# Kernel optimization log

Hardware: AMD Instinct MI355X
Metric: run time of the kernel (lower is better)

The kernel has to match this reference:

```python
import jax, jax.numpy as jnp
import numpy as np

N_NODES = 50000
N_EDGES = 800000
MUL = 32                      # multiplicity of 0e and 1o in node_feats
AVG_NUM_NEIGHBORS = 16.0
INV_SQRT3 = 1.0 / np.sqrt(3.0)


def setup_inputs() -> dict:
    key = jax.random.key(0)
    ks = jax.random.split(key, 7)
    return {
        "node_feats": jax.random.normal(ks[0], (N_NODES, 4 * MUL), dtype=jnp.float32),
        "edge_attrs": jax.random.normal(ks[1], (N_EDGES, 4), dtype=jnp.float32),
        "senders": jax.random.randint(ks[2], (N_EDGES,), 0, N_NODES, dtype=jnp.int64) if jax.config.jax_enable_x64 else jax.random.randint(ks[2], (N_EDGES,), 0, N_NODES, dtype=jnp.int32),
        "receivers": jax.random.randint(ks[3], (N_EDGES,), 0, N_NODES, dtype=jnp.int32),
        "w_mlp0": jax.random.normal(ks[4], (1, 64), dtype=jnp.float32),
        "w_mlp1": jax.random.normal(ks[5], (64, 64), dtype=jnp.float32),
        "w_mlp2": jax.random.normal(ks[6], (64, 4 * MUL), dtype=jnp.float32),
    }


def reference(node_feats, edge_attrs, senders, receivers, w_mlp0, w_mlp1, w_mlp2):
    # node_feats layout: [N, MUL] scalars (0e) then [N, MUL*3] flattened vectors (1o)
    s = node_feats[:, :MUL]                          # [N, MUL]   32x0e
    v = node_feats[:, MUL:].reshape(-1, MUL, 3)      # [N, MUL,3] 32x1o

    # gather sender features per edge
    s_e = s[senders]                                 # [E, MUL]
    v_e = v[senders]                                 # [E, MUL, 3]

    ea0 = edge_attrs[:, :1]                          # [E,1]  1x0e
    ea1 = edge_attrs[:, 1:4]                         # [E,3]  1x1o

    # equivariant tensor product with edge_attrs.filter(drop='0e') = 1x1o,
    # keeping only target irreps (0e,1o):
    #   0e x 1o -> 1o : scalar * vector
    tp_1o = s_e[:, :, None] * ea1[:, None, :]        # [E, MUL, 3]
    #   1o x 1o -> 0e : dot / sqrt(3)  (component normalization)
    tp_0e = jnp.einsum('eci,ei->ec', v_e, ea1) * INV_SQRT3  # [E, MUL]

    # concatenate([msgs.filter(target), tp]).regroup() -> 64x0e + 64x1o
    scalars = jnp.concatenate([s_e, tp_0e], axis=1)          # [E, 2*MUL]
    vectors = jnp.concatenate([v_e, tp_1o], axis=1)          # [E, 2*MUL, 3]

    # MLP gate on scalar edge attrs (e3nn MLP: no bias, 1/sqrt(fan_in), swish)
    h = jax.nn.swish(ea0 @ w_mlp0 / jnp.sqrt(1.0))           # [E,64]
    h = jax.nn.swish(h @ w_mlp1 / jnp.sqrt(64.0))            # [E,64]
    mix = h @ w_mlp2 / jnp.sqrt(64.0)                        # [E, 4*MUL]

    n_sc = 2 * MUL
    scalars = scalars * mix[:, :n_sc]                        # gate 0e
    vectors = vectors * mix[:, n_sc:, None]                  # gate 1o (one scalar per vector)

    msgs = jnp.concatenate([scalars, vectors.reshape(vectors.shape[0], -1)], axis=1)  # [E, 8*MUL]

    # scatter-add messages to receivers
    out = jax.ops.segment_sum(msgs, receivers, num_segments=N_NODES)  # [N, 8*MUL]
    return out / jnp.sqrt(AVG_NUM_NEIGHBORS)
```

## Files before the change

### kernel.cpp

```cpp
#include <hip/hip_runtime.h>
#include <hip/hip_fp16.h>
#include <cstdint>

#define N_NODES   50000
#define FEAT      128
#define OUTF      256
#define MAX_EDGES 800000
#define CAP       64
#define INV_SQRT3 0.57735026918962576f
#define NW        (64 + 64*64 + 64*128)
#define TB_BLKS   ((N_NODES * 32 + 255) / 256)

__device__ float    g_wf[NW];
__device__ uint16_t g_lut16[65536 * 128];
__device__ uint16_t g_tbl[N_NODES * FEAT];
__device__ int      g_flags[4];
__device__ int      g_cnt[N_NODES];
__device__ uint2    g_slot[N_NODES * CAP];
__device__ unsigned char g_used[65536];

__device__ __forceinline__ float b2f(uint32_t b) {
    union { uint32_t u; float f; } v; v.u = b << 16; return v.f;
}
__device__ __forceinline__ uint32_t f2b_bits(float f) {
    union { float f; uint32_t u; } v; v.f = f;
    uint32_t u = v.u;
    u += 0x7fffu + ((u >> 16) & 1u);
    return u >> 16;
}
__device__ __forceinline__ float swishf(float x) {
    return x / (1.0f + __expf(-x));
}
__device__ __forceinline__ float sane(float x) {
    union { float f; uint32_t u; } v; v.f = x;
    return (((v.u >> 23) & 0xffu) >= 0x8Du) ? 0.0f : x;
}
__device__ __forceinline__ float loadf(const void* p, int i, int isbf) {
    return isbf ? b2f(((const uint16_t*)p)[i]) : ((const float*)p)[i];
}
__device__ __forceinline__ float h2f(uint32_t bits16) {
    return __half2float(__ushort_as_half((unsigned short)bits16));
}
__device__ __forceinline__ uint32_t f2h(float x) {
    return (uint32_t)__half_as_ushort(__float2half(x));
}

__global__ __launch_bounds__(256) void init_kernel(
    const void* nf, const void* ea, const void* w0, const void* w1, const void* w2,
    const int* snd, const int* rcv, int snd_force64, int n_edges)
{
    int bx = blockIdx.x, t = threadIdx.x;
    if (bx == 0) {
        __shared__ int viol[4];
        if (t < 4) viol[t] = 0;
        __syncthreads();
        {   int n = N_NODES * FEAT; int step = (n / 256) | 1;
            long long i = (long long)t * step;
            if (i < n) {
                uint32_t e = (((const uint16_t*)nf)[i] >> 7) & 0xffu;
                if (e > 140u) atomicOr(&viol[2], 1);
            } }
        {   int n = n_edges * 4; int step = (n / 256) | 1;
            long long i = (long long)t * step;
            if (i < n) {
                uint32_t e = (((const uint16_t*)ea)[i] >> 7) & 0xffu;
                if (e > 140u) atomicOr(&viol[3], 1);
            } }
        if (t < 64) {
            int i = 2 * t + 1;
            if (i < 2 * n_edges) {
                if (snd[i] != 0) atomicOr(&viol[0], 1);
                if (rcv[i] != 0) atomicOr(&viol[1], 1);
            }
        }
        __syncthreads();
        if (t == 0) {
            g_flags[0] = snd_force64 ? 1 : !viol[0];
            g_flags[1] = !viol[1];
            g_flags[2] = !viol[2];
            g_flags[3] = !viol[3];
        }
    } else if (bx <= 49) {
        __shared__ int wv[3];
        if (t < 3) wv[t] = 0;
        __syncthreads();
        if (t < 64) {
            uint32_t e = (((const uint16_t*)w0)[t] >> 7) & 0xffu;
            if (e > 140u) atomicOr(&wv[0], 1);
        }
        { int i = t * 17; if (i < 4096) {
            uint32_t e = (((const uint16_t*)w1)[i] >> 7) & 0xffu;
            if (e > 140u) atomicOr(&wv[1], 1); } }
        { int i = t * 33; if (i < 8192) {
            uint32_t e = (((const uint16_t*)w2)[i] >> 7) & 0xffu;
            if (e > 140u) atomicOr(&wv[2], 1); } }
        __syncthreads();
        int i = (bx - 1) * 256 + t;
        if (i < 64)             g_wf[i] = loadf(w0, i, !wv[0]);
        else if (i < 64 + 4096) g_wf[i] = loadf(w1, i - 64, !wv[1]);
        else if (i < NW)        g_wf[i] = loadf(w2, i - (64 + 4096), !wv[2]);
    } else if (bx <= 49 + TB_BLKS) {
        __shared__ int nv;
        if (t == 0) nv = 0;
        __syncthreads();
        {   int n = N_NODES * FEAT; int step = (n / 256) | 1;
            long long i = (long long)t * step;
            if (i < n) {
                uint32_t e = (((const uint16_t*)nf)[i] >> 7) & 0xffu;
                if (e > 140u) atomicOr(&nv, 1);
            } }
        __syncthreads();
        int f2l = !nv;
        int i = (bx - 50) * 256 + t;
        if (i < N_NODES * 32) {
            int node = i >> 5, c = i & 31;
            int rb = node * FEAT;
            float s  = loadf(nf, rb + c, f2l);
            float v0 = loadf(nf, rb + 32 + 3 * c + 0, f2l);
            float v1 = loadf(nf, rb + 32 + 3 * c + 1, f2l);
            float v2 = loadf(nf, rb + 32 + 3 * c + 2, f2l);
            uint32_t lo = f2h(s)  | (f2h(v0) << 16);
            uint32_t hi = f2h(v1) | (f2h(v2) << 16);
            ((uint2*)g_tbl)[i] = make_uint2(lo, hi);
        }
    } else {
        __shared__ int ev[3];
        if (t < 3) ev[t] = 0;
        __syncthreads();
        {   int n = n_edges * 4; int step = (n / 256) | 1;
            long long i = (long long)t * step;
            if (i < n) {
                uint32_t x = (((const uint16_t*)ea)[i] >> 7) & 0xffu;
                if (x > 140u) atomicOr(&ev[2], 1);
            } }
        if (t < 64) {
            int i = 2 * t + 1;
            if (i < 2 * n_edges) {
                if (snd[i] != 0) atomicOr(&ev[0], 1);
                if (rcv[i] != 0) atomicOr(&ev[1], 1);
            }
        }
        __syncthreads();
        int f0l = snd_force64 ? 1 : !ev[0];
        int f1l = !ev[1];
        int f3l = !ev[2];
        int e = (bx - 50 - TB_BLKS) * 256 + t;
        if (e < n_edges) {
            int ri = f1l ? rcv[2 * e] : rcv[e];
            ri = min(max(ri, 0), N_NODES - 1);
            uint32_t b0 = f3l ? (uint32_t)((const uint16_t*)ea)[4 * e]
                              : f2b_bits(((const float*)ea)[4 * e]);
            b0 &= 0xffffu;
            int s_ = f0l ? snd[2 * e] : snd[e];
            s_ = min(max(s_, 0), N_NODES - 1);
            g_used[b0] = 1;
            int p = atomicAdd(&g_cnt[ri], 1);
            if (p < CAP) g_slot[ri * CAP + p] = make_uint2(((uint32_t)s_ << 16) | b0, (uint32_t)e);
        }
    }
}

__global__ __launch_bounds__(256) void lut_kernel() {
    int w = blockIdx.x * 4 + (threadIdx.x >> 6);
    int lane = threadIdx.x & 63;
    int f = (lane < 16) ? (g_used[w + lane * 4096] != 0) : 0;
    unsigned long long mask = __ballot(f) & 0xffffull;
    if (!mask) return;
    const float* w1 = g_wf + 64;
    const float* w2 = g_wf + 64 + 4096;
    float w0l = g_wf[lane];
    while (mask) {
        int k = __builtin_ctzll(mask);
        mask &= mask - 1;
        int r = w + k * 4096;
        float x = b2f((uint32_t)r);
        float h0 = swishf(x * w0l);
        float a = 0.f;
        #pragma unroll 8
        for (int kk = 0; kk < 64; ++kk)
            a += __shfl(h0, kk, 64) * w1[kk * 64 + lane];
        float h1 = swishf(a * 0.125f);
        float a0 = 0.f, a1 = 0.f;
        #pragma unroll 8
        for (int kk = 0; kk < 64; ++kk) {
            float h1k = __shfl(h1, kk, 64);
            a0 += h1k * w2[kk * 128 + lane];
            a1 += h1k * w2[kk * 128 + 64 + lane];
        }
        float s1c = 0.125f * 0.25f;
        float s0c = (lane >= 32) ? s1c * INV_SQRT3 : s1c;
        float pa = sane(a0 * s0c);
        float pb = sane(a1 * s1c);
        float qa = __shfl_xor(pa, 32, 64);
        float qb = __shfl_xor(pb, 32, 64);
        if (lane < 32) {
            uint32_t lo = f2h(pa) | (f2h(qa) << 16);
            uint32_t hi = f2h(pb) | (f2h(qb) << 16);
            ((uint2*)(g_lut16 + (size_t)r * 128))[lane] = make_uint2(lo, hi);
        }
    }
}

__global__ __launch_bounds__(256) void gather_kernel(
    const void* __restrict__ ea, void* __restrict__ out)
{
    int wid = (blockIdx.x * 256 + threadIdx.x) >> 6;
    int lane = threadIdx.x & 63;
    if (wid >= N_NODES) return;
    int c = lane & 31;
    int half = lane >> 5;
    const int f2 = g_flags[2], f3 = g_flags[3];
    int deg = min(g_cnt[wid], CAP);
    if (lane == 0) g_cnt[wid] = 0;

    float o0 = 0.f, o1 = 0.f, o2 = 0.f, o3 = 0.f,
          o4 = 0.f, o5 = 0.f, o6 = 0.f, o7 = 0.f;

    uint32_t pk_p = 0;
    float ex_p = 0.f, ey_p = 0.f, ez_p = 0.f;
    if (lane < deg) {
        uint2 sl = g_slot[wid * CAP + lane];
        pk_p = sl.x;
        int e = (int)sl.y;
        if (f3) {
            uint2 w = ((const uint2*)ea)[e];
            ex_p = b2f(w.x >> 16);
            ey_p = b2f(w.y & 0xffffu);
            ez_p = b2f(w.y >> 16);
        } else {
            float4 w = ((const float4*)ea)[e];
            ex_p = w.y; ey_p = w.z; ez_p = w.w;
        }
    }

    const uint2* tbl = (const uint2*)g_tbl;

    for (int j = 0; j < deg; j += 4) {
        int jjA = j + half, jjB = j + 2 + half;
        float gA = (jjA < deg) ? 1.0f : 0.0f;
        float gB = (jjB < deg) ? 1.0f : 0.0f;
        int jxA = (jjA < deg) ? jjA : 0;
        int jxB = (jjB < deg) ? jjB : 0;

        uint32_t pkA = (uint32_t)__shfl((int)pk_p, jxA, 64);
        uint32_t pkB = (uint32_t)__shfl((int)pk_p, jxB, 64);
        float exA = __shfl(ex_p, jxA, 64), eyA = __shfl(ey_p, jxA, 64), ezA = __shfl(ez_p, jxA, 64);
        float exB = __shfl(ex_p, jxB, 64), eyB = __shfl(ey_p, jxB, 64), ezB = __shfl(ez_p, jxB, 64);

        uint2 mAu = ((const uint2*)(g_lut16 + (size_t)(pkA & 0xffffu) * 128))[c];
        uint2 mBu = ((const uint2*)(g_lut16 + (size_t)(pkB & 0xffffu) * 128))[c];
        uint2 hA = tbl[(size_t)(pkA >> 16) * 32 + c];
        uint2 hB = tbl[(size_t)(pkB >> 16) * 32 + c];

        float sA  = h2f(hA.x & 0xffffu), vA0 = h2f(hA.x >> 16);
        float vA1 = h2f(hA.y & 0xffffu), vA2 = h2f(hA.y >> 16);
        float sB  = h2f(hB.x & 0xffffu), vB0 = h2f(hB.x >> 16);
        float vB1 = h2f(hB.y & 0xffffu), vB2 = h2f(hB.y >> 16);

        {
            float m0 = h2f(mAu.x & 0xffffu) * gA, m1 = h2f(mAu.x >> 16) * gA;
            float m2 = h2f(mAu.y & 0xffffu) * gA, m3 = h2f(mAu.y >> 16) * gA;
            o0 += sA * m0;
            o1 += (vA0 * exA + vA1 * eyA + vA2 * ezA) * m1;
            o2 += vA0 * m2; o3 += vA1 * m2; o4 += vA2 * m2;
            float sm3 = sA * m3;
            o5 += exA * sm3; o6 += eyA * sm3; o7 += ezA * sm3;
        }
        {
            float m0 = h2f(mBu.x & 0xffffu) * gB, m1 = h2f(mBu.x >> 16) * gB;
            float m2 = h2f(mBu.y & 0xffffu) * gB, m3 = h2f(mBu.y >> 16) * gB;
            o0 += sB * m0;
            o1 += (vB0 * exB + vB1 * eyB + vB2 * ezB) * m1;
            o2 += vB0 * m2; o3 += vB1 * m2; o4 += vB2 * m2;
            float sm3 = sB * m3;
            o5 += exB * sm3; o6 += eyB * sm3; o7 += ezB * sm3;
        }
    }

    o0 += __shfl_xor(o0, 32, 64);
    o1 += __shfl_xor(o1, 32, 64);
    o2 += __shfl_xor(o2, 32, 64);
    o3 += __shfl_xor(o3, 32, 64);
    o4 += __shfl_xor(o4, 32, 64);
    o5 += __shfl_xor(o5, 32, 64);
    o6 += __shfl_xor(o6, 32, 64);
    o7 += __shfl_xor(o7, 32, 64);

    if (half == 0) {
        size_t bo = (size_t)wid * OUTF;
        if (f2) {
            uint16_t* o = (uint16_t*)out;
            o[bo + c]             = (uint16_t)f2b_bits(o0);
            o[bo + 32 + c]        = (uint16_t)f2b_bits(o1);
            o[bo + 64 + 3*c + 0]  = (uint16_t)f2b_bits(o2);
            o[bo + 64 + 3*c + 1]  = (uint16_t)f2b_bits(o3);
            o[bo + 64 + 3*c + 2]  = (uint16_t)f2b_bits(o4);
            o[bo + 160 + 3*c + 0] = (uint16_t)f2b_bits(o5);
            o[bo + 160 + 3*c + 1] = (uint16_t)f2b_bits(o6);
            o[bo + 160 + 3*c + 2] = (uint16_t)f2b_bits(o7);
        } else {
            float* o = (float*)out;
            o[bo + c]             = o0;
            o[bo + 32 + c]        = o1;
            o[bo + 64 + 3*c + 0]  = o2;
            o[bo + 64 + 3*c + 1]  = o3;
            o[bo + 64 + 3*c + 2]  = o4;
            o[bo + 160 + 3*c + 0] = o5;
            o[bo + 160 + 3*c + 1] = o6;
            o[bo + 160 + 3*c + 2] = o7;
        }
    }
}

extern "C" void kernel_launch(void* const* d_in, const int* in_sizes, int n_in,
                              void* d_out, int out_size, void* d_ws, size_t ws_size,
                              hipStream_t stream) {
    (void)n_in; (void)out_size; (void)d_ws; (void)ws_size;
    const void* nf = d_in[0];
    const void* ea = d_in[1];
    const int* snd = (const int*)d_in[2];
    const int* rcv = (const int*)d_in[3];
    const void* w0 = d_in[4];
    const void* w1 = d_in[5];
    const void* w2 = d_in[6];

    int n_edges = in_sizes[1] / 4;
    if (n_edges > MAX_EDGES) n_edges = MAX_EDGES;
    int snd_force64 = (in_sizes[2] == 2 * in_sizes[3]) ? 1 : 0;
    int eb = (n_edges + 255) / 256;

    init_kernel<<<50 + TB_BLKS + eb, 256, 0, stream>>>(nf, ea, w0, w1, w2, snd, rcv, snd_force64, n_edges);
    lut_kernel<<<1024, 256, 0, stream>>>();
    gather_kernel<<<(N_NODES + 3) / 4, 256, 0, stream>>>(ea, d_out);
}
```

Before: 215.2 us.

## Shrink edge slots to indices, load sender and bucket in gather, stage MLP weights in LDS

The bucketing pass now stores only the edge index (4 bytes) per receiver slot, using a nontemporal store instead of the 8-byte packed sender/bucket pair. The gather kernel reloads the sender and the bf16 bucket key from the inputs and packs them itself. This halves slot traffic but adds scattered sender reads in gather. The LUT kernel also stages the two MLP weight matrices in shared memory before evaluating its buckets. The gather path reads the sender-width flag from g_flags[0], and the init code that sets g_flags is not shown, so it is unclear whether that flag is still written correctly.

```diff
diff --git a/kernel.cpp b/kernel.cpp
--- a/kernel.cpp
+++ b/kernel.cpp
@@ -16,7 +16,7 @@
 __device__ uint16_t g_tbl[N_NODES * FEAT];
 __device__ int      g_flags[4];
 __device__ int      g_cnt[N_NODES];
-__device__ uint2    g_slot[N_NODES * CAP];
+__device__ uint32_t g_slot[N_NODES * CAP];
 __device__ unsigned char g_used[65536];
 
 __device__ __forceinline__ float b2f(uint32_t b) {
@@ -124,50 +124,49 @@
             ((uint2*)g_tbl)[i] = make_uint2(lo, hi);
         }
     } else {
-        __shared__ int ev[3];
-        if (t < 3) ev[t] = 0;
+        __shared__ int ev[2];
+        if (t < 2) ev[t] = 0;
         __syncthreads();
         {   int n = n_edges * 4; int step = (n / 256) | 1;
             long long i = (long long)t * step;
             if (i < n) {
                 uint32_t x = (((const uint16_t*)ea)[i] >> 7) & 0xffu;
-                if (x > 140u) atomicOr(&ev[2], 1);
+                if (x > 140u) atomicOr(&ev[1], 1);
             } }
         if (t < 64) {
             int i = 2 * t + 1;
             if (i < 2 * n_edges) {
-                if (snd[i] != 0) atomicOr(&ev[0], 1);
-                if (rcv[i] != 0) atomicOr(&ev[1], 1);
+                if (rcv[i] != 0) atomicOr(&ev[0], 1);
             }
         }
         __syncthreads();
-        int f0l = snd_force64 ? 1 : !ev[0];
-        int f1l = !ev[1];
-        int f3l = !ev[2];
+        int f1l = !ev[0];
+        int f3l = !ev[1];
         int e = (bx - 50 - TB_BLKS) * 256 + t;
         if (e < n_edges) {
             int ri = f1l ? rcv[2 * e] : rcv[e];
             ri = min(max(ri, 0), N_NODES - 1);
             uint32_t b0 = f3l ? (uint32_t)((const uint16_t*)ea)[4 * e]
                               : f2b_bits(((const float*)ea)[4 * e]);
-            b0 &= 0xffffu;
-            int s_ = f0l ? snd[2 * e] : snd[e];
-            s_ = min(max(s_, 0), N_NODES - 1);
-            g_used[b0] = 1;
+            g_used[b0 & 0xffffu] = 1;
             int p = atomicAdd(&g_cnt[ri], 1);
-            if (p < CAP) g_slot[ri * CAP + p] = make_uint2(((uint32_t)s_ << 16) | b0, (uint32_t)e);
+            if (p < CAP) __builtin_nontemporal_store((uint32_t)e, &g_slot[ri * CAP + p]);
         }
     }
 }
 
 __global__ __launch_bounds__(256) void lut_kernel() {
+    __shared__ float sw[4096 + 8192];
     int w = blockIdx.x * 4 + (threadIdx.x >> 6);
     int lane = threadIdx.x & 63;
+    for (int i = threadIdx.x; i < 4096 + 8192; i += 256)
+        sw[i] = g_wf[64 + i];
     int f = (lane < 16) ? (g_used[w + lane * 4096] != 0) : 0;
     unsigned long long mask = __ballot(f) & 0xffffull;
+    __syncthreads();
     if (!mask) return;
-    const float* w1 = g_wf + 64;
-    const float* w2 = g_wf + 64 + 4096;
+    const float* w1 = sw;
+    const float* w2 = sw + 4096;
     float w0l = g_wf[lane];
     while (mask) {
         int k = __builtin_ctzll(mask);
@@ -202,14 +201,14 @@
 }
 
 __global__ __launch_bounds__(256) void gather_kernel(
-    const void* __restrict__ ea, void* __restrict__ out)
+    const void* __restrict__ ea, const int* __restrict__ snd, void* __restrict__ out)
 {
     int wid = (blockIdx.x * 256 + threadIdx.x) >> 6;
     int lane = threadIdx.x & 63;
     if (wid >= N_NODES) return;
     int c = lane & 31;
     int half = lane >> 5;
-    const int f2 = g_flags[2], f3 = g_flags[3];
+    const int f0 = g_flags[0], f2 = g_flags[2], f3 = g_flags[3];
     int deg = min(g_cnt[wid], CAP);
     if (lane == 0) g_cnt[wid] = 0;
 
@@ -219,18 +218,22 @@
     uint32_t pk_p = 0;
     float ex_p = 0.f, ey_p = 0.f, ez_p = 0.f;
     if (lane < deg) {
-        uint2 sl = g_slot[wid * CAP + lane];
-        pk_p = sl.x;
-        int e = (int)sl.y;
+        uint32_t e = __builtin_nontemporal_load(&g_slot[wid * CAP + lane]);
+        uint32_t b0;
         if (f3) {
             uint2 w = ((const uint2*)ea)[e];
+            b0 = w.x & 0xffffu;
             ex_p = b2f(w.x >> 16);
             ey_p = b2f(w.y & 0xffffu);
             ez_p = b2f(w.y >> 16);
         } else {
             float4 w = ((const float4*)ea)[e];
+            b0 = f2b_bits(w.x) & 0xffffu;
             ex_p = w.y; ey_p = w.z; ez_p = w.w;
         }
+        int s_ = f0 ? snd[2 * e] : snd[e];
+        s_ = min(max(s_, 0), N_NODES - 1);
+        pk_p = ((uint32_t)s_ << 16) | b0;
     }
 
     const uint2* tbl = (const uint2*)g_tbl;
@@ -331,5 +334,5 @@
 
     init_kernel<<<50 + TB_BLKS + eb, 256, 0, stream>>>(nf, ea, w0, w1, w2, snd, rcv, snd_force64, n_edges);
     lut_kernel<<<1024, 256, 0, stream>>>();
-    gather_kernel<<<(N_NODES + 3) / 4, 256, 0, stream>>>(ea, d_out);
-}
+    gather_kernel<<<(N_NODES + 3) / 4, 256, 0, stream>>>(ea, snd, d_out);
+}
```

Measured after the change: 243.8 us. 1.13x slower.

## Reschedule prep work: overlap LUT build with edge bucketing and node table conversion

Applied to the files above, without the earlier changes.

Moves the edge bucketing (atomic slot insertion) and the node feature fp16 table conversion out of the init kernel into a new prep kernel that also builds the MLP lookup table. The init kernel now only zeroes counts, converts weights and marks used edge-attribute keys, so the LUT build, bucketing and table conversion can share one launch and overlap. It also unrolls the LUT dot products with multiple accumulators and moves count reset from gather to init. The sender 64-bit force flag is dropped in prep, which could misread senders when the int64 check is wrong.

```diff
diff --git a/kernel.cpp b/kernel.cpp
--- a/kernel.cpp
+++ b/kernel.cpp
@@ -80,7 +80,10 @@
             g_flags[2] = !viol[2];
             g_flags[3] = !viol[3];
         }
-    } else if (bx <= 49) {
+    } else if (bx <= 196) {
+        int i = (bx - 1) * 256 + t;
+        if (i < N_NODES) g_cnt[i] = 0;
+    } else if (bx <= 245) {
         __shared__ int wv[3];
         if (t < 3) wv[t] = 0;
         __syncthreads();
@@ -95,12 +98,131 @@
             uint32_t e = (((const uint16_t*)w2)[i] >> 7) & 0xffu;
             if (e > 140u) atomicOr(&wv[2], 1); } }
         __syncthreads();
-        int i = (bx - 1) * 256 + t;
+        int i = (bx - 197) * 256 + t;
         if (i < 64)             g_wf[i] = loadf(w0, i, !wv[0]);
         else if (i < 64 + 4096) g_wf[i] = loadf(w1, i - 64, !wv[1]);
         else if (i < NW)        g_wf[i] = loadf(w2, i - (64 + 4096), !wv[2]);
-    } else if (bx <= 49 + TB_BLKS) {
+    } else {
+        __shared__ int viol;
+        if (t == 0) viol = 0;
+        __syncthreads();
+        {
+            int n = n_edges * 4; int step = (n / 256) | 1;
+            long long i = (long long)t * step;
+            if (i < n) {
+                uint32_t e = (((const uint16_t*)ea)[i] >> 7) & 0xffu;
+                if (e > 140u) atomicOr(&viol, 1);
+            }
+        }
+        __syncthreads();
+        int f3l = !viol;
+        int e = (bx - 246) * 256 + t;
+        if (e < n_edges) {
+            uint32_t b0 = f3l ? (uint32_t)((const uint16_t*)ea)[4 * e]
+                              : f2b_bits(((const float*)ea)[4 * e]);
+            b0 &= 0xffffu;
+            if (!g_used[b0]) g_used[b0] = 1;
+        }
+    }
+}
+
+__global__ __launch_bounds__(256) void prep_kernel(
+    const void* __restrict__ nf, const void* __restrict__ ea,
+    const int* __restrict__ snd, const int* __restrict__ rcv,
+    int n_edges, int eb)
+{
+    int bx = blockIdx.x;
+    if (bx < 1024) {
+        int w = bx * 4 + (threadIdx.x >> 6);
+        int lane = threadIdx.x & 63;
+        int f = (lane < 16) ? (g_used[w + lane * 4096] != 0) : 0;
+        unsigned long long mask = __ballot(f) & 0xffffull;
+        if (!mask) return;
+        const float* w1 = g_wf + 64;
+        const float* w2 = g_wf + 64 + 4096;
+        float w0l = g_wf[lane];
+        while (mask) {
+            int k = __builtin_ctzll(mask);
+            mask &= mask - 1;
+            int r = w + k * 4096;
+            float x = b2f((uint32_t)r);
+            float h0 = swishf(x * w0l);
+            float aa0 = 0.f, aa1 = 0.f, aa2 = 0.f, aa3 = 0.f;
+            #pragma unroll
+            for (int kk = 0; kk < 64; kk += 4) {
+                aa0 += __shfl(h0, kk + 0, 64) * w1[(kk + 0) * 64 + lane];
+                aa1 += __shfl(h0, kk + 1, 64) * w1[(kk + 1) * 64 + lane];
+                aa2 += __shfl(h0, kk + 2, 64) * w1[(kk + 2) * 64 + lane];
+                aa3 += __shfl(h0, kk + 3, 64) * w1[(kk + 3) * 64 + lane];
+            }
+            float h1 = swishf(((aa0 + aa1) + (aa2 + aa3)) * 0.125f);
+            float b00 = 0.f, b01 = 0.f, b10 = 0.f, b11 = 0.f;
+            float b02 = 0.f, b03 = 0.f, b12 = 0.f, b13 = 0.f;
+            #pragma unroll
+            for (int kk = 0; kk < 64; kk += 2) {
+                float hk0 = __shfl(h1, kk, 64);
+                float hk1 = __shfl(h1, kk + 1, 64);
+                b00 += hk0 * w2[kk * 128 + lane];
+                b02 += hk0 * w2[kk * 128 + 64 + lane];
+                b01 += hk1 * w2[(kk + 1) * 128 + lane];
+                b03 += hk1 * w2[(kk + 1) * 128 + 64 + lane];
+                (void)b10; (void)b11; (void)b12; (void)b13;
+            }
+            float a0 = b00 + b01;
+            float a1 = b02 + b03;
+            float s1c = 0.125f * 0.25f;
+            float s0c = (lane >= 32) ? s1c * INV_SQRT3 : s1c;
+            float pa = sane(a0 * s0c);
+            float pb = sane(a1 * s1c);
+            float qa = __shfl_xor(pa, 32, 64);
+            float qb = __shfl_xor(pb, 32, 64);
+            if (lane < 32) {
+                uint32_t lo = f2h(pa) | (f2h(qa) << 16);
+                uint32_t hi = f2h(pb) | (f2h(qb) << 16);
+                ((uint2*)(g_lut16 + (size_t)r * 128))[lane] = make_uint2(lo, hi);
+            }
+        }
+    } else if (bx < 1024 + eb) {
+        __shared__ int ev[3];
+        int t = threadIdx.x;
+        if (t < 3) ev[t] = 0;
+        __syncthreads();
+        {   int n = n_edges * 4; int step = (n / 256) | 1;
+            long long i = (long long)t * step;
+            if (i < n) {
+                uint32_t x = (((const uint16_t*)ea)[i] >> 7) & 0xffu;
+                if (x > 140u) atomicOr(&ev[2], 1);
+            } }
+        if (t < 64) {
+            int i = 2 * t + 1;
+            if (i < 2 * n_edges) {
+                if (snd[i] != 0) atomicOr(&ev[0], 1);
+                if (rcv[i] != 0) atomicOr(&ev[1], 1);
+            }
+        }
+        __syncthreads();
+        int f0l = ev[0] ? 0 : 1;
+        f0l = !ev[0];
+        int f1l = !ev[1];
+        int f3l = !ev[2];
+        int e = (bx - 1024) * 256 + t;
+        if (e >= n_edges) return;
+        int ri = f1l ? rcv[2 * e] : rcv[e];
+        ri = min(max(ri, 0), N_NODES - 1);
+        uint32_t b0;
+        if (f3l) {
+            b0 = (uint32_t)((const uint16_t*)ea)[4 * e];
+        } else {
+            b0 = f2b_bits(((const float*)ea)[4 * e]);
+        }
+        b0 &= 0xffffu;
+        int s_ = f0l ? snd[2 * e] : snd[e];
+        s_ = min(max(s_, 0), N_NODES - 1);
+        int p = atomicAdd(&g_cnt[ri], 1);
+        if (p < CAP) g_slot[ri * CAP + p] = make_uint2(((uint32_t)s_ << 16) | b0, (uint32_t)e);
+    } else {
         __shared__ int nv;
+        int t = threadIdx.x;
         if (t == 0) nv = 0;
         __syncthreads();
         {   int n = N_NODES * FEAT; int step = (n / 256) | 1;
@@ -111,7 +233,7 @@
             } }
         __syncthreads();
         int f2l = !nv;
-        int i = (bx - 50) * 256 + t;
+        int i = (bx - 1024 - eb) * 256 + t;
         if (i < N_NODES * 32) {
             int node = i >> 5, c = i & 31;
             int rb = node * FEAT;
@@ -123,81 +245,6 @@
             uint32_t hi = f2h(v1) | (f2h(v2) << 16);
             ((uint2*)g_tbl)[i] = make_uint2(lo, hi);
         }
-    } else {
-        __shared__ int ev[3];
-        if (t < 3) ev[t] = 0;
-        __syncthreads();
-        {   int n = n_edges * 4; int step = (n / 256) | 1;
-            long long i = (long long)t * step;
-            if (i < n) {
-                uint32_t x = (((const uint16_t*)ea)[i] >> 7) & 0xffu;
-                if (x > 140u) atomicOr(&ev[2], 1);
-            } }
-        if (t < 64) {
-            int i = 2 * t + 1;
-            if (i < 2 * n_edges) {
-                if (snd[i] != 0) atomicOr(&ev[0], 1);
-                if (rcv[i] != 0) atomicOr(&ev[1], 1);
-            }
-        }
-        __syncthreads();
-        int f0l = snd_force64 ? 1 : !ev[0];
-        int f1l = !ev[1];
-        int f3l = !ev[2];
-        int e = (bx - 50 - TB_BLKS) * 256 + t;
-        if (e < n_edges) {
-            int ri = f1l ? rcv[2 * e] : rcv[e];
-            ri = min(max(ri, 0), N_NODES - 1);
-            uint32_t b0 = f3l ? (uint32_t)((const uint16_t*)ea)[4 * e]
-                              : f2b_bits(((const float*)ea)[4 * e]);
-            b0 &= 0xffffu;
-            int s_ = f0l ? snd[2 * e] : snd[e];
-            s_ = min(max(s_, 0), N_NODES - 1);
-            g_used[b0] = 1;
-            int p = atomicAdd(&g_cnt[ri], 1);
-            if (p < CAP) g_slot[ri * CAP + p] = make_uint2(((uint32_t)s_ << 16) | b0, (uint32_t)e);
-        }
-    }
-}
-
-__global__ __launch_bounds__(256) void lut_kernel() {
-    int w = blockIdx.x * 4 + (threadIdx.x >> 6);
-    int lane = threadIdx.x & 63;
-    int f = (lane < 16) ? (g_used[w + lane * 4096] != 0) : 0;
-    unsigned long long mask = __ballot(f) & 0xffffull;
-    if (!mask) return;
-    const float* w1 = g_wf + 64;
-    const float* w2 = g_wf + 64 + 4096;
-    float w0l = g_wf[lane];
-    while (mask) {
-        int k = __builtin_ctzll(mask);
-        mask &= mask - 1;
-        int r = w + k * 4096;
-        float x = b2f((uint32_t)r);
-        float h0 = swishf(x * w0l);
-        float a = 0.f;
-        #pragma unroll 8
-        for (int kk = 0; kk < 64; ++kk)
-            a += __shfl(h0, kk, 64) * w1[kk * 64 + lane];
-        float h1 = swishf(a * 0.125f);
-        float a0 = 0.f, a1 = 0.f;
-        #pragma unroll 8
-        for (int kk = 0; kk < 64; ++kk) {
-            float h1k = __shfl(h1, kk, 64);
-            a0 += h1k * w2[kk * 128 + lane];
-            a1 += h1k * w2[kk * 128 + 64 + lane];
-        }
-        float s1c = 0.125f * 0.25f;
-        float s0c = (lane >= 32) ? s1c * INV_SQRT3 : s1c;
-        float pa = sane(a0 * s0c);
-        float pb = sane(a1 * s1c);
-        float qa = __shfl_xor(pa, 32, 64);
-        float qb = __shfl_xor(pb, 32, 64);
-        if (lane < 32) {
-            uint32_t lo = f2h(pa) | (f2h(qa) << 16);
-            uint32_t hi = f2h(pb) | (f2h(qb) << 16);
-            ((uint2*)(g_lut16 + (size_t)r * 128))[lane] = make_uint2(lo, hi);
-        }
     }
 }
 
@@ -211,7 +258,6 @@
     int half = lane >> 5;
     const int f2 = g_flags[2], f3 = g_flags[3];
     int deg = min(g_cnt[wid], CAP);
-    if (lane == 0) g_cnt[wid] = 0;
 
     float o0 = 0.f, o1 = 0.f, o2 = 0.f, o3 = 0.f,
           o4 = 0.f, o5 = 0.f, o6 = 0.f, o7 = 0.f;
@@ -329,7 +375,7 @@
     int snd_force64 = (in_sizes[2] == 2 * in_sizes[3]) ? 1 : 0;
     int eb = (n_edges + 255) / 256;
 
-    init_kernel<<<50 + TB_BLKS + eb, 256, 0, stream>>>(nf, ea, w0, w1, w2, snd, rcv, snd_force64, n_edges);
-    lut_kernel<<<1024, 256, 0, stream>>>();
+    init_kernel<<<246 + eb, 256, 0, stream>>>(nf, ea, w0, w1, w2, snd, rcv, snd_force64, n_edges);
+    prep_kernel<<<1024 + eb + TB_BLKS, 256, 0, stream>>>(nf, ea, snd, rcv, n_edges, eb);
     gather_kernel<<<(N_NODES + 3) / 4, 256, 0, stream>>>(ea, d_out);
 }
```

Result: slower. 240.3 us (+11.7%).
